# Performance work log

Measured on AMD Instinct MI355X. Metric: run time of the kernel, lower is better.

## Reference

```python
import jax, jax.numpy as jnp
import numpy as np

E = 5        # num_experts
K = 2        # top-k routing
DIM = 768    # token dim
HID = 3072   # dim * mlp_ratio
T = 16384    # num tokens (batch*seq collapsed, per SparseDispatcher contract)
EPS = float(np.finfo(np.float64).eps)  # np.finfo(float).eps used in combine


def setup_inputs() -> dict:
    key = jax.random.key(0)
    ks = jax.random.split(key, 5)
    x = jax.random.normal(ks[0], (T, DIM), jnp.float32)
    # w_gate is nn.Parameter(zeros) in the source; randomize so routing is non-trivial
    w_gate = jax.random.normal(ks[1], (DIM, E), jnp.float32) * 0.02
    # stacked ExpertMLP params (fc1: dim->hid, fc2: hid->dim), small init per init_weights
    W1 = jax.random.normal(ks[2], (E, DIM, HID), jnp.float32) * 0.02
    b1 = jnp.zeros((E, HID), jnp.float32)
    W2 = jax.random.normal(ks[3], (E, HID, DIM), jnp.float32) * 0.02
    b2 = jnp.zeros((E, DIM), jnp.float32)
    return {"x": x, "w_gate": w_gate, "W1": W1, "b1": b1, "W2": W2, "b2": b2}


def reference(x, w_gate, W1, b1, W2, b2):
    # --- noisy top-k gating, eval mode (no noise added at inference) ---
    logits = x @ w_gate                              # [T, E]
    top_vals, top_idx = jax.lax.top_k(logits, K)     # [T, K]
    top_gates = jax.nn.softmax(top_vals, axis=-1)    # softmax over selected logits
    tok = jnp.arange(x.shape[0])[:, None]
    gates = jnp.zeros_like(logits).at[tok, top_idx].set(top_gates)  # sparse [T, E]

    # --- dispatch / expert MLP / combine ---
    # SparseDispatcher.combine: combined[b] = log(sum_e gate[b,e] * exp(expert_e(x[b])))
    # (zeros where no expert contributes are replaced by eps before log)
    acc = jnp.zeros((x.shape[0], DIM), jnp.float32)
    for e in range(E):  # small fixed expert count; dense-equivalent of sparse dispatch
        h = jax.nn.gelu(x @ W1[e] + b1[e], approximate=False)  # torch nn.GELU (erf)
        y = h @ W2[e] + b2[e]                                   # [T, DIM]
        acc = acc + gates[:, e:e + 1] * jnp.exp(y)
    return jnp.log(jnp.where(acc == 0.0, EPS, acc))
```

## Files before the change

### kernel.cpp

```cpp
#include <hip/hip_runtime.h>
#include <math.h>

#define T_TOK 16384
#define DIM   768
#define HID   3072
#define NE    5
#define MT    65
#define HCAP  (MT * 128)
#define CSTR  32
#define EPSF  2.2204460492503131e-16f

typedef short bf16x8  __attribute__((ext_vector_type(8)));
typedef float f32x4   __attribute__((ext_vector_type(4)));
typedef float f32x16  __attribute__((ext_vector_type(16)));

#define MFMA16(A, B, C) __builtin_amdgcn_mfma_f32_16x16x32_bf16((A), (B), (C), 0, 0, 0)
#define MFMA32(A, B, C) __builtin_amdgcn_mfma_f32_32x32x16_bf16((A), (B), (C), 0, 0, 0)

__device__ __forceinline__ unsigned short f2bf(float f) {
    unsigned int u = __float_as_uint(f);
    unsigned int r = (u + 0x7fffu + ((u >> 16) & 1u)) >> 16;
    return (unsigned short)r;
}

__device__ __forceinline__ void gld16(const void* g, void* l) {
    __builtin_amdgcn_global_load_lds(
        (const __attribute__((address_space(1))) void*)g,
        (__attribute__((address_space(3))) void*)l, 16, 0, 0);
}

__device__ __forceinline__ int xcd_swz(int orig, int nwg) {
    int q = nwg >> 3, r = nwg & 7;
    int xcd = orig & 7, off = orig >> 3;
    int base = (xcd < r) ? xcd * (q + 1) : r * (q + 1) + (xcd - r) * q;
    return base + off;
}

__global__ void prep_w1p(const float* __restrict__ W1, unsigned short* __restrict__ W1p) {
    int idx = blockIdx.x * 256 + threadIdx.x;
    if (idx >= NE * 24 * 12 * 128 * 8) return;
    int p = idx & 7;
    int n = (idx >> 3) & 127;
    int t = idx >> 10;
    int kb = t % 12; t /= 12;
    int nb = t % 24; int e = t / 24;
    int klog = kb * 64 + (p ^ (n & 7)) * 8;
    const float* src = W1 + ((size_t)e * DIM + klog) * HID + nb * 128 + n;
    bf16x8 v;
    #pragma unroll
    for (int j = 0; j < 8; ++j) v[j] = (short)f2bf(src[(size_t)j * HID]);
    *reinterpret_cast<bf16x8*>(W1p + (size_t)idx * 8) = v;
}

__global__ void prep_w2p(const float* __restrict__ W2, unsigned short* __restrict__ W2p) {
    int idx = blockIdx.x * 256 + threadIdx.x;
    if (idx >= NE * 6 * 48 * 128 * 8) return;
    int p = idx & 7;
    int n = (idx >> 3) & 127;
    int t = idx >> 10;
    int kb = t % 48; t /= 48;
    int nb = t % 6; int e = t / 6;
    int klog = kb * 64 + (p ^ (n & 7)) * 8;
    const float* src = W2 + ((size_t)e * HID + klog) * DIM + nb * 128 + n;
    bf16x8 v;
    #pragma unroll
    for (int j = 0; j < 8; ++j) v[j] = (short)f2bf(src[(size_t)j * DIM]);
    *reinterpret_cast<bf16x8*>(W2p + (size_t)idx * 8) = v;
}

__global__ __launch_bounds__(256) void gate_kernel(
    const float* __restrict__ x, const float* __restrict__ wg,
    unsigned short* __restrict__ xb, int* __restrict__ counts,
    int* __restrict__ btok, float* __restrict__ bgate) {
    __shared__ int   s_e[2][64];
    __shared__ float s_g[2][64];
    __shared__ int   lcnt[NE];
    __shared__ int   gbase[NE];

    const int tid = threadIdx.x;
    if (tid < NE) lcnt[tid] = 0;
    const int grp = tid >> 4, l16 = tid & 15;
    const int t0 = blockIdx.x * 64 + grp * 4;

    double acc[4][NE];
    #pragma unroll
    for (int tt = 0; tt < 4; ++tt)
        #pragma unroll
        for (int e = 0; e < NE; ++e) acc[tt][e] = 0.0;

    for (int i = 0; i < 12; ++i) {
        const int dbase = i * 64 + l16 * 4;
        float4 xv[4];
        #pragma unroll
        for (int tt = 0; tt < 4; ++tt) {
            xv[tt] = *reinterpret_cast<const float4*>(x + (size_t)(t0 + tt) * DIM + dbase);
            ushort4 o;
            o.x = f2bf(xv[tt].x); o.y = f2bf(xv[tt].y);
            o.z = f2bf(xv[tt].z); o.w = f2bf(xv[tt].w);
            *reinterpret_cast<ushort4*>(xb + (size_t)(t0 + tt) * DIM + dbase) = o;
        }
        #pragma unroll
        for (int j = 0; j < 4; ++j) {
            const int d = dbase + j;
            float w0 = wg[d * NE + 0], w1 = wg[d * NE + 1], w2 = wg[d * NE + 2];
            float w3 = wg[d * NE + 3], w4 = wg[d * NE + 4];
            #pragma unroll
            for (int tt = 0; tt < 4; ++tt) {
                double xd = (double)((&xv[tt].x)[j]);
                acc[tt][0] += xd * (double)w0;
                acc[tt][1] += xd * (double)w1;
                acc[tt][2] += xd * (double)w2;
                acc[tt][3] += xd * (double)w3;
                acc[tt][4] += xd * (double)w4;
            }
        }
    }
    #pragma unroll
    for (int off = 8; off; off >>= 1)
        #pragma unroll
        for (int tt = 0; tt < 4; ++tt)
            #pragma unroll
            for (int e = 0; e < NE; ++e)
                acc[tt][e] += __shfl_down(acc[tt][e], off, 16);

    if (l16 == 0) {
        #pragma unroll
        for (int tt = 0; tt < 4; ++tt) {
            double v[NE] = {acc[tt][0], acc[tt][1], acc[tt][2], acc[tt][3], acc[tt][4]};
            int i0 = 0;
            for (int e = 1; e < NE; ++e) if (v[e] > v[i0]) i0 = e;
            int i1 = -1;
            for (int e = 0; e < NE; ++e) {
                if (e == i0) continue;
                if (i1 < 0 || v[e] > v[i1]) i1 = e;
            }
            float e1 = expf((float)(v[i1] - v[i0]));
            float g0 = 1.0f / (1.0f + e1);
            int li = grp * 4 + tt;
            s_e[0][li] = i0;  s_g[0][li] = g0;
            s_e[1][li] = i1;  s_g[1][li] = e1 * g0;
        }
    }
    __syncthreads();

    int mye = 0, myoff = 0, mytok = 0;
    float myg = 0.0f;
    if (tid < 128) {
        int li = tid >> 1, which = tid & 1;
        mye = s_e[which][li];
        myg = s_g[which][li];
        mytok = blockIdx.x * 64 + li;
        myoff = atomicAdd(&lcnt[mye], 1);
    }
    __syncthreads();
    if (tid < NE) gbase[tid] = atomicAdd(&counts[tid * CSTR], lcnt[tid]);
    __syncthreads();
    if (tid < 128) {
        int p = gbase[mye] + myoff;
        btok[mye * T_TOK + p] = mytok;
        bgate[mye * T_TOK + p] = myg;
    }
}

__global__ __launch_bounds__(256, 4) void combo_kernel(
    const unsigned short* __restrict__ xb,
    const unsigned short* __restrict__ W1p,
    const unsigned short* __restrict__ W2p,
    const float* __restrict__ b1, const float* __restrict__ b2,
    const int* __restrict__ counts, const int* __restrict__ btok,
    const float* __restrict__ bgate,
    unsigned short* __restrict__ hall, int slotmask,
    float* __restrict__ out, int g1s, int g1n, int g2s, int g2n) {
    __shared__ __align__(16) unsigned short As[128 * 64];
    __shared__ __align__(16) unsigned short Bs[128 * 64];
    __shared__ int   sst[128];
    __shared__ float ssg[128];

    const int g2seg = MT * 6, g1seg = MT * 24;
    int bx = blockIdx.x;
    const int g2tot = g2n * g2seg;
    const bool isG2 = bx < g2tot;
    int e, mt, nt;
    if (isG2) {
        e = g2s + bx / g2seg;
        int w = xcd_swz(bx % g2seg, g2seg);
        mt = w / 6;  nt = w % 6;
    } else {
        bx -= g2tot;
        e = g1s + bx / g1seg;
        int w = xcd_swz(bx % g1seg, g1seg);
        mt = w / 24; nt = w % 24;
    }
    const int cnt = counts[e * CSTR];
    const int m0 = mt * 128;
    if (m0 >= cnt) return;
    unsigned short* hbuf = hall + (size_t)(e & slotmask) * ((size_t)HCAP * HID);

    const int tid = threadIdx.x;
    const int wv = tid >> 6, lane = tid & 63;
    const int wm = wv >> 1, wn = wv & 1;
    const int col = lane & 15, quad = lane >> 4;
    const int l8 = lane & 7, r8 = lane >> 3;

    const unsigned short* aptr[4];
    if (isG2) {
        if (tid < 128) {
            int pos = m0 + tid;
            sst[tid] = (pos < cnt) ? btok[e * T_TOK + pos] : 0;
            ssg[tid] = (pos < cnt) ? bgate[e * T_TOK + pos] : 0.0f;
        }
        #pragma unroll
        for (int q = 0; q < 4; ++q) {
            int r = wv * 32 + q * 8 + r8;
            aptr[q] = hbuf + (size_t)(m0 + r) * HID + (l8 ^ r8) * 8;
        }
    } else {
        #pragma unroll
        for (int q = 0; q < 4; ++q) {
            int r = wv * 32 + q * 8 + r8;
            int pos = m0 + r;
            int tok = btok[e * T_TOK + (pos < cnt ? pos : 0)];
            aptr[q] = xb + (size_t)tok * DIM + (l8 ^ r8) * 8;
        }
    }
    const unsigned short* btile = isG2
        ? W2p + ((size_t)(e * 6 + nt)) * 48 * 8192
        : W1p + ((size_t)(e * 24 + nt)) * 12 * 8192;
    const int ksteps = isG2 ? 48 : 12;

    f32x4 acc[4][4];
    #pragma unroll
    for (int i = 0; i < 4; ++i)
        #pragma unroll
        for (int j = 0; j < 4; ++j)
            acc[i][j] = (f32x4){0.f, 0.f, 0.f, 0.f};

    for (int ks = 0; ks < ksteps; ++ks) {
        const unsigned short* bk = btile + (size_t)ks * 8192 + (size_t)wv * 2048 + lane * 8;
        #pragma unroll
        for (int q = 0; q < 4; ++q)
            gld16(aptr[q] + ks * 64, &As[(wv * 4 + q) * 512]);
        #pragma unroll
        for (int q = 0; q < 4; ++q)
            gld16(bk + q * 512, &Bs[(wv * 4 + q) * 512]);
        __syncthreads();
        #pragma unroll
        for (int kf = 0; kf < 2; ++kf) {
            const int p = ((kf * 4 + quad) ^ l8) * 8;
            bf16x8 a[4], b[4];
            #pragma unroll
            for (int i = 0; i < 4; ++i)
                a[i] = *reinterpret_cast<const bf16x8*>(&As[(wm * 64 + i * 16 + col) * 64 + p]);
            #pragma unroll
            for (int i = 0; i < 4; ++i)
                b[i] = *reinterpret_cast<const bf16x8*>(&Bs[(wn * 64 + i * 16 + col) * 64 + p]);
            #pragma unroll
            for (int i = 0; i < 4; ++i)
                #pragma unroll
                for (int j = 0; j < 4; ++j)
                    acc[i][j] = MFMA16(a[i], b[j], acc[i][j]);
        }
        __syncthreads();
    }

    const int nb0 = nt * 128 + wn * 64;
    if (!isG2) {
        #pragma unroll
        for (int j = 0; j < 4; ++j) {
            float bias = b1[e * HID + nb0 + j * 16 + col];
            #pragma unroll
            for (int i = 0; i < 4; ++i) {
                #pragma unroll
                for (int r = 0; r < 4; ++r) {
                    int row = m0 + wm * 64 + i * 16 + quad * 4 + r;
                    float v = acc[i][j][r] + bias;
                    float gl = 0.5f * v * (1.0f + erff(v * 0.70710678118654752f));
                    hbuf[(size_t)row * HID + nb0 + j * 16 + col] = f2bf(gl);
                }
            }
        }
    } else {
        #pragma unroll
        for (int j = 0; j < 4; ++j) {
            float bias = b2[e * DIM + nb0 + j * 16 + col];
            #pragma unroll
            for (int i = 0; i < 4; ++i) {
                #pragma unroll
                for (int r = 0; r < 4; ++r) {
                    int lrow = wm * 64 + i * 16 + quad * 4 + r;
                    float g = ssg[lrow];
                    if (g > 0.0f) {
                        float v = acc[i][j][r] + bias;
                        atomicAdd(out + (size_t)sst[lrow] * DIM + nb0 + j * 16 + col,
                                  g * expf(v));
                    }
                }
            }
        }
    }
}

__global__ void log_kernel(float* __restrict__ out, int n) {
    int i = blockIdx.x * 256 + threadIdx.x;
    if (i < n) {
        float v = out[i];
        out[i] = logf(v == 0.0f ? EPSF : v);
    }
}

__global__ void prep_w1_v2(const float* __restrict__ W1, unsigned short* __restrict__ W1s) {
    int g = blockIdx.x * 4 + (threadIdx.x >> 6);
    int lane = threadIdx.x & 63;
    int kf = g % 48;
    int rest = g / 48;
    int nt2 = rest % 96;
    int e = rest / 96;
    int n = nt2 * 32 + (lane & 31);
    int k0 = kf * 16 + (lane >> 5) * 8;
    const float* src = W1 + ((size_t)e * DIM + k0) * HID + n;
    bf16x8 v;
    #pragma unroll
    for (int j = 0; j < 8; ++j) v[j] = (short)f2bf(src[(size_t)j * HID]);
    *reinterpret_cast<bf16x8*>(W1s + ((size_t)g * 64 + lane) * 8) = v;
}

__global__ void prep_w2_v2(const float* __restrict__ W2, unsigned short* __restrict__ W2s) {
    int g = blockIdx.x * 4 + (threadIdx.x >> 6);
    int lane = threadIdx.x & 63;
    int kf = g % 192;
    int rest = g / 192;
    int nt2 = rest % 24;
    int e = rest / 24;
    int n = nt2 * 32 + (lane & 31);
    int k0 = kf * 16 + (lane >> 5) * 8;
    const float* src = W2 + ((size_t)e * HID + k0) * DIM + n;
    bf16x8 v;
    #pragma unroll
    for (int j = 0; j < 8; ++j) v[j] = (short)f2bf(src[(size_t)j * DIM]);
    *reinterpret_cast<bf16x8*>(W2s + ((size_t)g * 64 + lane) * 8) = v;
}

__global__ __launch_bounds__(512, 2) void expert_v2(
    const unsigned short* __restrict__ xb, const unsigned short* __restrict__ W1s,
    const unsigned short* __restrict__ W2s, const float* __restrict__ b1,
    const float* __restrict__ b2, const int* __restrict__ counts,
    const int* __restrict__ btok, const float* __restrict__ bgate,
    float* __restrict__ out) {
    __shared__ __align__(16) unsigned short xs[64][776];
    __shared__ __align__(16) unsigned short hs[2][64][136];
    __shared__ int   st[64];
    __shared__ float sg[64];

    const int e = blockIdx.y;
    const int cnt = counts[e * CSTR];
    const int m0 = blockIdx.x * 64;
    if (m0 >= cnt) return;

    const int tid = threadIdx.x;
    const int wv = tid >> 6, lane = tid & 63;
    const int l31 = lane & 31, lhi = lane >> 5;

    if (tid < 64) {
        int pos = m0 + tid;
        st[tid] = (pos < cnt) ? btok[e * T_TOK + pos] : 0;
        sg[tid] = (pos < cnt) ? bgate[e * T_TOK + pos] : 0.0f;
    }
    __syncthreads();
    {
        int r = tid >> 3, seg = tid & 7;
        const unsigned short* src = xb + (size_t)st[r] * DIM + seg * 96;
        unsigned short* dst = &xs[r][seg * 96];
        #pragma unroll
        for (int i = 0; i < 12; ++i)
            reinterpret_cast<bf16x8*>(dst)[i] = reinterpret_cast<const bf16x8*>(src)[i];
    }
    __syncthreads();

    const int mt2 = wv & 1, nt2l = wv >> 1;
    f32x16 acc[2][3];
    #pragma unroll
    for (int a_ = 0; a_ < 2; ++a_)
        #pragma unroll
        for (int b_ = 0; b_ < 3; ++b_)
            #pragma unroll
            for (int q = 0; q < 16; ++q) acc[a_][b_][q] = 0.0f;

    const unsigned short* arow = &xs[mt2 * 32 + l31][lhi * 8];
    for (int jc = 0; jc < 24; ++jc) {
        f32x16 c0, c1;
        #pragma unroll
        for (int q = 0; q < 16; ++q) { c0[q] = 0.0f; c1[q] = 0.0f; }
        const unsigned short* bpa =
            W1s + ((size_t)((e * 96 + jc * 4 + nt2l) * 48)) * 512 + lane * 8;
        #pragma unroll
        for (int kf = 0; kf < 48; kf += 2) {
            bf16x8 a0 = *reinterpret_cast<const bf16x8*>(arow + kf * 16);
            bf16x8 b0 = *reinterpret_cast<const bf16x8*>(bpa + (size_t)kf * 512);
            c0 = MFMA32(a0, b0, c0);
            bf16x8 a1 = *reinterpret_cast<const bf16x8*>(arow + kf * 16 + 16);
            bf16x8 b1 = *reinterpret_cast<const bf16x8*>(bpa + (size_t)kf * 512 + 512);
            c1 = MFMA32(a1, b1, c1);
        }
        #pragma unroll
        for (int q = 0; q < 16; ++q) c0[q] += c1[q];
        {
            int colc = nt2l * 32 + l31;
            float bias = b1[e * HID + jc * 128 + colc];
            #pragma unroll
            for (int reg = 0; reg < 16; ++reg) {
                int row = (reg & 3) + 8 * (reg >> 2) + 4 * lhi;
                float v = c0[reg] + bias;
                float gl = 0.5f * v * (1.0f + erff(v * 0.70710678118654752f));
                hs[jc & 1][mt2 * 32 + row][colc] = f2bf(gl);
            }
        }
        __syncthreads();
        const unsigned short* bpb =
            W2s + ((size_t)((e * 24 + wv * 3) * 192 + jc * 8)) * 512 + lane * 8;
        #pragma unroll
        for (int kf = 0; kf < 8; ++kf) {
            bf16x8 af0 = *reinterpret_cast<const bf16x8*>(&hs[jc & 1][l31][kf * 16 + lhi * 8]);
            bf16x8 af1 = *reinterpret_cast<const bf16x8*>(&hs[jc & 1][32 + l31][kf * 16 + lhi * 8]);
            #pragma unroll
            for (int i = 0; i < 3; ++i) {
                bf16x8 bv = *reinterpret_cast<const bf16x8*>(bpb + ((size_t)i * 192 + kf) * 512);
                acc[0][i] = MFMA32(af0, bv, acc[0][i]);
                acc[1][i] = MFMA32(af1, bv, acc[1][i]);
            }
        }
    }
    #pragma unroll
    for (int mt = 0; mt < 2; ++mt) {
        #pragma unroll
        for (int i = 0; i < 3; ++i) {
            int cg = (wv * 3 + i) * 32 + l31;
            float bias2 = b2[e * DIM + cg];
            #pragma unroll
            for (int reg = 0; reg < 16; ++reg) {
                int row = mt * 32 + (reg & 3) + 8 * (reg >> 2) + 4 * lhi;
                float g = sg[row];
                if (g > 0.0f) {
                    float v = acc[mt][i][reg] + bias2;
                    atomicAdd(out + (size_t)st[row] * DIM + cg, g * expf(v));
                }
            }
        }
    }
}


extern "C" void kernel_launch(void* const* d_in, const int* in_sizes, int n_in,
                              void* d_out, int out_size, void* d_ws, size_t ws_size,
                              hipStream_t stream) {
    const float* x  = (const float*)d_in[0];
    const float* wg = (const float*)d_in[1];
    const float* W1 = (const float*)d_in[2];
    const float* b1 = (const float*)d_in[3];
    const float* W2 = (const float*)d_in[4];
    const float* b2 = (const float*)d_in[5];
    float* out = (float*)d_out;

    char* ws = (char*)d_ws;
    int*            counts = (int*)ws;
    int*            btok   = (int*)(ws + 1024);
    float*          bgate  = (float*)(ws + 1024 + 327680);
    unsigned short* xb     = (unsigned short*)(ws + 1024 + 2 * 327680);
    unsigned short* W1b    = xb + (size_t)T_TOK * DIM;
    unsigned short* W2b    = W1b + (size_t)NE * DIM * HID;
    unsigned short* hall   = W2b + (size_t)NE * HID * DIM;

    const size_t HBsh  = (size_t)HCAP * HID;
    const size_t fixed = 1024 + 2 * 327680
        + (size_t)T_TOK * DIM * 2 + 2 * (size_t)NE * DIM * HID * 2;
    auto need = [&](int k) { return fixed + (size_t)k * HBsh * 2; };

    const int g1seg = MT * 24, g2seg = MT * 6;

    hipMemsetAsync(counts, 0, 1024, stream);
    hipMemsetAsync(out, 0, (size_t)out_size * sizeof(float), stream);

    gate_kernel<<<T_TOK / 64, 256, 0, stream>>>(x, wg, xb, counts, btok, bgate);

    if (ws_size >= need(2)) {
        prep_w1p<<<(NE * 24 * 12 * 128 * 8 + 255) / 256, 256, 0, stream>>>(W1, W1b);
        prep_w2p<<<(NE * 6 * 48 * 128 * 8 + 255) / 256, 256, 0, stream>>>(W2, W2b);

        auto launch_combo = [&](int g1s, int g1n, int g2s, int g2n, int slotmask) {
            int nb = g1n * g1seg + g2n * g2seg;
            if (nb <= 0) return;
            combo_kernel<<<nb, 256, 0, stream>>>(xb, W1b, W2b, b1, b2, counts,
                                                 btok, bgate, hall, slotmask, out,
                                                 g1s, g1n, g2s, g2n);
        };

        if (ws_size >= need(5)) {
            launch_combo(0, 5, 0, 0, 7);
            launch_combo(0, 0, 0, 5, 7);
        } else if (ws_size >= need(4)) {
            launch_combo(0, 2, 0, 0, 3);
            launch_combo(2, 2, 0, 1, 3);
            launch_combo(4, 1, 1, 2, 3);
            launch_combo(0, 0, 3, 2, 3);
        } else {
            for (int s = 0; s < 6; ++s)
                launch_combo(s, (s <= 4) ? 1 : 0, s - 1, (s >= 1) ? 1 : 0, 1);
        }
    } else {
        prep_w1_v2<<<NE * 96 * 48 / 4, 256, 0, stream>>>(W1, W1b);
        prep_w2_v2<<<NE * 24 * 192 / 4, 256, 0, stream>>>(W2, W2b);
        expert_v2<<<dim3(T_TOK / 64, NE), 512, 0, stream>>>(
            xb, W1b, W2b, b1, b2, counts, btok, bgate, out);
    }

    log_kernel<<<(out_size + 255) / 256, 256, 0, stream>>>(out, out_size);
}
```

Before: 719.0 us.

## Enlarge combo GEMM tiles to 256x256 with double-buffered async LDS staging

Result: slower. 1.017 ms (+41.4%).

```diff
diff --git a/kernel.cpp b/kernel.cpp
--- a/kernel.cpp
+++ b/kernel.cpp
@@ -5,8 +5,8 @@
 #define DIM   768
 #define HID   3072
 #define NE    5
-#define MT    65
-#define HCAP  (MT * 128)
+#define MT3   32
+#define HCAP  8320
 #define CSTR  32
 #define EPSF  2.2204460492503131e-16f
 
@@ -162,7 +162,7 @@
     }
 }
 
-__global__ __launch_bounds__(256, 4) void combo_kernel(
+__global__ __launch_bounds__(512, 2) void combo_kernel(
     const unsigned short* __restrict__ xb,
     const unsigned short* __restrict__ W1p,
     const unsigned short* __restrict__ W2p,
@@ -171,12 +171,12 @@
     const float* __restrict__ bgate,
     unsigned short* __restrict__ hall, int slotmask,
     float* __restrict__ out, int g1s, int g1n, int g2s, int g2n) {
-    __shared__ __align__(16) unsigned short As[128 * 64];
-    __shared__ __align__(16) unsigned short Bs[128 * 64];
-    __shared__ int   sst[128];
-    __shared__ float ssg[128];
-
-    const int g2seg = MT * 6, g1seg = MT * 24;
+    __shared__ __align__(16) unsigned short As[2][256 * 64];
+    __shared__ __align__(16) unsigned short Bs[2][256 * 64];
+    __shared__ int   sst[256];
+    __shared__ float ssg[256];
+
+    const int g2seg = MT3 * 3, g1seg = MT3 * 12;
     int bx = blockIdx.x;
     const int g2tot = g2n * g2seg;
     const bool isG2 = bx < g2tot;
@@ -184,27 +184,28 @@
     if (isG2) {
         e = g2s + bx / g2seg;
         int w = xcd_swz(bx % g2seg, g2seg);
-        mt = w / 6;  nt = w % 6;
+        mt = w / 3;  nt = w % 3;
     } else {
         bx -= g2tot;
         e = g1s + bx / g1seg;
         int w = xcd_swz(bx % g1seg, g1seg);
-        mt = w / 24; nt = w % 24;
+        mt = w / 12; nt = w % 12;
     }
     const int cnt = counts[e * CSTR];
-    const int m0 = mt * 128;
+    const int m0 = mt * 256;
     if (m0 >= cnt) return;
     unsigned short* hbuf = hall + (size_t)(e & slotmask) * ((size_t)HCAP * HID);
 
     const int tid = threadIdx.x;
     const int wv = tid >> 6, lane = tid & 63;
-    const int wm = wv >> 1, wn = wv & 1;
+    const int wm = wv >> 2, wn = wv & 3;
     const int col = lane & 15, quad = lane >> 4;
     const int l8 = lane & 7, r8 = lane >> 3;
+    const int ksteps = isG2 ? 48 : 12;
 
     const unsigned short* aptr[4];
     if (isG2) {
-        if (tid < 128) {
+        if (tid < 256) {
             int pos = m0 + tid;
             sst[tid] = (pos < cnt) ? btok[e * T_TOK + pos] : 0;
             ssg[tid] = (pos < cnt) ? bgate[e * T_TOK + pos] : 0.0f;
@@ -224,55 +225,75 @@
         }
     }
     const unsigned short* btile = isG2
-        ? W2p + ((size_t)(e * 6 + nt)) * 48 * 8192
-        : W1p + ((size_t)(e * 24 + nt)) * 12 * 8192;
-    const int ksteps = isG2 ? 48 : 12;
-
-    f32x4 acc[4][4];
-    #pragma unroll
-    for (int i = 0; i < 4; ++i)
+        ? W2p + ((size_t)(e * 6 + nt * 2)) * 48 * 8192
+        : W1p + ((size_t)(e * 24 + nt * 2)) * 12 * 8192;
+    const unsigned short* bsrc = btile
+        + (size_t)(wv >> 2) * ((size_t)ksteps * 8192)
+        + (size_t)((wv & 3) * 4) * 512 + lane * 8;
+
+    auto STAGE = [&](int KS, int B_) {
+        #pragma unroll
+        for (int q = 0; q < 4; ++q)
+            gld16(aptr[q] + KS * 64, &As[B_][(wv * 4 + q) * 512]);
+        #pragma unroll
+        for (int q = 0; q < 4; ++q)
+            gld16(bsrc + (size_t)KS * 8192 + q * 512, &Bs[B_][(wv * 4 + q) * 512]);
+    };
+
+    f32x4 acc[8][4];
+    #pragma unroll
+    for (int i = 0; i < 8; ++i)
         #pragma unroll
         for (int j = 0; j < 4; ++j)
             acc[i][j] = (f32x4){0.f, 0.f, 0.f, 0.f};
 
-    for (int ks = 0; ks < ksteps; ++ks) {
-        const unsigned short* bk = btile + (size_t)ks * 8192 + (size_t)wv * 2048 + lane * 8;
-        #pragma unroll
-        for (int q = 0; q < 4; ++q)
-            gld16(aptr[q] + ks * 64, &As[(wv * 4 + q) * 512]);
-        #pragma unroll
-        for (int q = 0; q < 4; ++q)
-            gld16(bk + q * 512, &Bs[(wv * 4 + q) * 512]);
-        __syncthreads();
+    auto COMPUTE = [&](int B_) {
         #pragma unroll
         for (int kf = 0; kf < 2; ++kf) {
             const int p = ((kf * 4 + quad) ^ l8) * 8;
-            bf16x8 a[4], b[4];
-            #pragma unroll
-            for (int i = 0; i < 4; ++i)
-                a[i] = *reinterpret_cast<const bf16x8*>(&As[(wm * 64 + i * 16 + col) * 64 + p]);
-            #pragma unroll
-            for (int i = 0; i < 4; ++i)
-                b[i] = *reinterpret_cast<const bf16x8*>(&Bs[(wn * 64 + i * 16 + col) * 64 + p]);
-            #pragma unroll
-            for (int i = 0; i < 4; ++i)
+            bf16x8 a[8], b[4];
+            #pragma unroll
+            for (int i = 0; i < 8; ++i)
+                a[i] = *reinterpret_cast<const bf16x8*>(&As[B_][(wm * 128 + i * 16 + col) * 64 + p]);
+            #pragma unroll
+            for (int j = 0; j < 4; ++j)
+                b[j] = *reinterpret_cast<const bf16x8*>(&Bs[B_][(wn * 64 + j * 16 + col) * 64 + p]);
+            #pragma unroll
+            for (int i = 0; i < 8; ++i)
                 #pragma unroll
                 for (int j = 0; j < 4; ++j)
                     acc[i][j] = MFMA16(a[i], b[j], acc[i][j]);
         }
-        __syncthreads();
-    }
-
-    const int nb0 = nt * 128 + wn * 64;
+    };
+
+    STAGE(0, 0);
+    STAGE(1, 1);
+    for (int ks = 0; ks < ksteps; ++ks) {
+        if (ks + 1 < ksteps)
+            asm volatile("s_waitcnt vmcnt(8)" ::: "memory");
+        else
+            asm volatile("s_waitcnt vmcnt(0)" ::: "memory");
+        __builtin_amdgcn_s_barrier();
+        asm volatile("" ::: "memory");
+        __builtin_amdgcn_s_setprio(1);
+        COMPUTE(ks & 1);
+        __builtin_amdgcn_s_setprio(0);
+        asm volatile("" ::: "memory");
+        __builtin_amdgcn_s_barrier();
+        asm volatile("" ::: "memory");
+        if (ks + 2 < ksteps) STAGE(ks + 2, ks & 1);
+    }
+
+    const int nb0 = nt * 256 + wn * 64;
     if (!isG2) {
         #pragma unroll
         for (int j = 0; j < 4; ++j) {
             float bias = b1[e * HID + nb0 + j * 16 + col];
             #pragma unroll
-            for (int i = 0; i < 4; ++i) {
+            for (int i = 0; i < 8; ++i) {
                 #pragma unroll
                 for (int r = 0; r < 4; ++r) {
-                    int row = m0 + wm * 64 + i * 16 + quad * 4 + r;
+                    int row = m0 + wm * 128 + i * 16 + quad * 4 + r;
                     float v = acc[i][j][r] + bias;
                     float gl = 0.5f * v * (1.0f + erff(v * 0.70710678118654752f));
                     hbuf[(size_t)row * HID + nb0 + j * 16 + col] = f2bf(gl);
@@ -284,10 +305,10 @@
         for (int j = 0; j < 4; ++j) {
             float bias = b2[e * DIM + nb0 + j * 16 + col];
             #pragma unroll
-            for (int i = 0; i < 4; ++i) {
+            for (int i = 0; i < 8; ++i) {
                 #pragma unroll
                 for (int r = 0; r < 4; ++r) {
-                    int lrow = wm * 64 + i * 16 + quad * 4 + r;
+                    int lrow = wm * 128 + i * 16 + quad * 4 + r;
                     float g = ssg[lrow];
                     if (g > 0.0f) {
                         float v = acc[i][j][r] + bias;
@@ -474,7 +495,7 @@
         + (size_t)T_TOK * DIM * 2 + 2 * (size_t)NE * DIM * HID * 2;
     auto need = [&](int k) { return fixed + (size_t)k * HBsh * 2; };
 
-    const int g1seg = MT * 24, g2seg = MT * 6;
+    const int g1seg = MT3 * 12, g2seg = MT3 * 3;
 
     hipMemsetAsync(counts, 0, 1024, stream);
     hipMemsetAsync(out, 0, (size_t)out_size * sizeof(float), stream);
@@ -488,7 +509,7 @@
         auto launch_combo = [&](int g1s, int g1n, int g2s, int g2n, int slotmask) {
             int nb = g1n * g1seg + g2n * g2seg;
             if (nb <= 0) return;
-            combo_kernel<<<nb, 256, 0, stream>>>(xb, W1b, W2b, b1, b2, counts,
+            combo_kernel<<<nb, 512, 0, stream>>>(xb, W1b, W2b, b1, b2, counts,
                                                  btok, bgate, hall, slotmask, out,
                                                  g1s, g1n, g2s, g2n);
         };
```

## Stage GEMM epilogues through LDS for coalesced vector stores, drop atomics

Applied to the files above, without the earlier changes.

Measured after the change: 658.4 us. -8.4%, faster.

```diff
diff --git a/kernel.cpp b/kernel.cpp
--- a/kernel.cpp
+++ b/kernel.cpp
@@ -265,37 +265,64 @@
 
     const int nb0 = nt * 128 + wn * 64;
     if (!isG2) {
-        #pragma unroll
-        for (int j = 0; j < 4; ++j) {
-            float bias = b1[e * HID + nb0 + j * 16 + col];
-            #pragma unroll
-            for (int i = 0; i < 4; ++i) {
+        unsigned short (*X)[128] = reinterpret_cast<unsigned short (*)[128]>(As);
+        #pragma unroll
+        for (int i = 0; i < 4; ++i) {
+            #pragma unroll
+            for (int j = 0; j < 4; ++j) {
+                float bias = b1[e * HID + nb0 + j * 16 + col];
                 #pragma unroll
                 for (int r = 0; r < 4; ++r) {
-                    int row = m0 + wm * 64 + i * 16 + quad * 4 + r;
                     float v = acc[i][j][r] + bias;
                     float gl = 0.5f * v * (1.0f + erff(v * 0.70710678118654752f));
-                    hbuf[(size_t)row * HID + nb0 + j * 16 + col] = f2bf(gl);
+                    X[wm * 16 + quad * 4 + r][wn * 64 + j * 16 + col] = f2bf(gl);
                 }
             }
+            __syncthreads();
+            {
+                int lr = tid >> 3, g = tid & 7;
+                int grow = m0 + (lr >> 4) * 64 + i * 16 + (lr & 15);
+                unsigned short* dst = hbuf + (size_t)grow * HID + nt * 128;
+                *reinterpret_cast<bf16x8*>(dst + g * 8) =
+                    *reinterpret_cast<const bf16x8*>(&X[lr][g * 8]);
+                *reinterpret_cast<bf16x8*>(dst + 64 + g * 8) =
+                    *reinterpret_cast<const bf16x8*>(&X[lr][64 + g * 8]);
+            }
+            __syncthreads();
         }
     } else {
-        #pragma unroll
-        for (int j = 0; j < 4; ++j) {
-            float bias = b2[e * DIM + nb0 + j * 16 + col];
-            #pragma unroll
-            for (int i = 0; i < 4; ++i) {
+        float (*Xf)[128] = reinterpret_cast<float (*)[128]>(As);
+        #pragma unroll
+        for (int i = 0; i < 4; ++i) {
+            #pragma unroll
+            for (int j = 0; j < 4; ++j) {
+                float bias = b2[e * DIM + nb0 + j * 16 + col];
                 #pragma unroll
                 for (int r = 0; r < 4; ++r) {
                     int lrow = wm * 64 + i * 16 + quad * 4 + r;
                     float g = ssg[lrow];
-                    if (g > 0.0f) {
-                        float v = acc[i][j][r] + bias;
-                        atomicAdd(out + (size_t)sst[lrow] * DIM + nb0 + j * 16 + col,
-                                  g * expf(v));
+                    float v = acc[i][j][r] + bias;
+                    Xf[wm * 16 + quad * 4 + r][wn * 64 + j * 16 + col] =
+                        (g > 0.0f) ? g * expf(v) : 0.0f;
+                }
+            }
+            __syncthreads();
+            {
+                int lr = tid >> 3, gq = tid & 7;
+                int lrow = (lr >> 4) * 64 + i * 16 + (lr & 15);
+                if (m0 + lrow < cnt) {
+                    float* dst = out + (size_t)sst[lrow] * DIM + nt * 128 + gq * 16;
+                    const float* src = &Xf[lr][gq * 16];
+                    #pragma unroll
+                    for (int q = 0; q < 4; ++q) {
+                        float4 o = *reinterpret_cast<float4*>(dst + q * 4);
+                        float4 a = *reinterpret_cast<const float4*>(src + q * 4);
+                        o.x += a.x; o.y += a.y; o.z += a.z; o.w += a.w;
+                        *reinterpret_cast<float4*>(dst + q * 4) = o;
                     }
                 }
             }
+            __syncthreads();
         }
     }
 }
```
